# Optimization experiments

Measured on AMD Instinct MI355X. Metric: run time of the kernel, lower is better.

The kernel has to match this reference:

```python
import jax, jax.numpy as jnp
import numpy as np

# nqsystems=8 grouped sites, physical dim d=2^ncontraq=16,
# state bond r=64, layer (unitary MPO) bond rl=16, operator MPO bond ro=4,
# nlsystems=1 pre-contracted circuit layer.
NQ, R, D, RL, RO, NL = 8, 64, 16, 16, 4, 1


def setup_inputs() -> dict:
    key = jax.random.key(0)
    k1, k2, k3 = jax.random.split(key, 3)
    # scale so contractions stay O(1) numerically
    state = jax.random.normal(k1, (NQ, R, D, R), jnp.float32) / np.float32(np.sqrt(R * D))
    layer = jax.random.normal(k2, (NL, NQ, RL, D, D, RL), jnp.float32) / np.float32(np.sqrt(RL * D))
    operator = jax.random.normal(k3, (NQ, RO, D, D, RO), jnp.float32) / np.float32(np.sqrt(RO * D))
    return {"state": state, "layer": layer, "operator": operator}


def reference(state, layer, operator):
    """<psi| U^dagger O U |psi> contracted site-by-site along the TT chain.

    state:    [nq, r, d, r]        TT cores of |psi>
    layer:    [nl, nq, rl, d, d, rl]  TT-operator cores of the circuit layer (nl=1)
    operator: [nq, ro, d, d, ro]   TT-operator cores of the observable
    """
    r, rl, ro = state.shape[1], layer.shape[3], operator.shape[1]
    # open-boundary closure: boundary vectors = e0 on every bond
    env0 = jnp.zeros((r, rl, ro, rl, r), state.dtype).at[0, 0, 0, 0, 0].set(1.0)
    U = layer[0]  # nlsystems == 1

    def step(env, cores):
        S, Uq, Oq = cores
        # tt_dagger: conj + transpose physical indices (0,2,1,3)
        Ud = jnp.conj(Uq).transpose(0, 2, 1, 3)
        # env axes: a=bra-state bond, l=bra-layer bond, o=operator bond,
        #           m=ket-layer bond, b=ket-state bond
        t = jnp.einsum('alomb,aiA->lombiA', env, jnp.conj(S))   # bra state core
        t = jnp.einsum('lombiA,lijL->ombAjL', t, Ud)            # U^dagger core
        t = jnp.einsum('ombAjL,ojkO->mbALkO', t, Oq)            # observable core
        t = jnp.einsum('mbALkO,mksM->bALOsM', t, Uq)            # U core
        t = jnp.einsum('bALOsM,bsB->ALOMB', t, S)               # ket state core
        return t, None

    env, _ = jax.lax.scan(step, env0, (state, U, operator))
    return env[0, 0, 0, 0, 0]
```

## Files before the change

### kernel.cpp

```cpp
#include <hip/hip_runtime.h>


typedef __attribute__((ext_vector_type(8))) short bf16x8;
typedef __attribute__((ext_vector_type(8))) _Float16 f16x8;
typedef __attribute__((ext_vector_type(4))) float f32x4;
typedef __attribute__((ext_vector_type(4))) unsigned short us4;

static __device__ __forceinline__ unsigned short f2bf(float x) {
    union { float f; unsigned u; } a; a.f = x;
    return (unsigned short)((a.u + 0x7FFF + ((a.u >> 16) & 1)) >> 16);
}
static __device__ __forceinline__ float bf2f(unsigned short h) {
    union { unsigned u; float f; } a; a.u = (unsigned)h << 16; return a.f;
}
static __device__ __forceinline__ unsigned split2(float x) {
    unsigned short h = f2bf(x);
    unsigned short l = f2bf(x - bf2f(h));
    return (unsigned)h | ((unsigned)l << 16);
}
static __device__ __forceinline__ void split2_pair(float x0, float x1,
                                                   unsigned& o0, unsigned& o1) {
    unsigned hh, ll;
    asm("v_cvt_pk_bf16_f32 %0, %1, %2" : "=v"(hh) : "v"(x0), "v"(x1));
    union { unsigned u; float f; } c0, c1;
    c0.u = hh << 16;
    c1.u = hh & 0xffff0000u;
    float r0 = x0 - c0.f, r1 = x1 - c1.f;
    asm("v_cvt_pk_bf16_f32 %0, %1, %2" : "=v"(ll) : "v"(r0), "v"(r1));
    asm("v_perm_b32 %0, %1, %2, %3" : "=v"(o0) : "v"(ll), "v"(hh), "s"(0x05040100));
    asm("v_perm_b32 %0, %1, %2, %3" : "=v"(o1) : "v"(ll), "v"(hh), "s"(0x07060302));
}
static __device__ __forceinline__ unsigned short f2h_bits(float x) {
    union { _Float16 h; unsigned short u; } c; c.h = (_Float16)x; return c.u;
}
static __device__ __forceinline__ float h2f_bits(unsigned short u) {
    union { unsigned short u; _Float16 h; } c; c.u = u; return (float)c.h;
}
static __device__ __forceinline__ void gl_lds16(const unsigned short* g,
                                                unsigned short* l) {
    __builtin_amdgcn_global_load_lds(
        (const __attribute__((address_space(1))) unsigned int*)g,
        (__attribute__((address_space(3))) unsigned int*)l, 16, 0, 0);
}

__global__ void write_diag_kernel(float* out, float v) {
    if (threadIdx.x == 0 && blockIdx.x == 0) out[0] = v;
}
__global__ void zero_out(float* o) {
    if (threadIdx.x == 0 && blockIdx.x == 0) o[0] = 0.0f;
}

__global__ void prep_apack(const float* __restrict__ layer,
                           unsigned short* __restrict__ Ap2,
                           unsigned short* __restrict__ Ap4) {
    int idx = blockIdx.x * 256 + threadIdx.x;
    int q = idx >> 13, k0 = (idx >> 10) & 7, mt = (idx >> 6) & 15, lane = idx & 63;
    int quad = lane >> 4, r = lane & 15;
    unsigned short h2[8], l2[8], h4[8], l4[8];
#pragma unroll
    for (int j = 0; j < 8; j++) {
        int k = k0 * 32 + quad * 8 + j;
        int m = mt * 16 + r;
        float v2 = layer[(size_t)q * 65536 +
                         (size_t)((((k >> 4) * 16 + (m >> 4)) * 16 + (k & 15)) * 16 + (m & 15))];
        float v4 = layer[(size_t)q * 65536 +
                         (size_t)((((k >> 4) * 16 + (k & 15)) * 16 + (m >> 4)) * 16 + (m & 15))];
        h2[j] = f2h_bits(v2); l2[j] = f2h_bits(v2 - h2f_bits(h2[j]));
        h4[j] = f2h_bits(v4); l4[j] = f2h_bits(v4 - h2f_bits(h4[j]));
    }
    size_t base = ((size_t)((q * 8 + k0) * 16 + mt) * 2) * 512 + lane * 8;
    *(us4*)(Ap2 + base)       = *(us4*)&h2[0];
    *(us4*)(Ap2 + base + 4)   = *(us4*)&h2[4];
    *(us4*)(Ap2 + base + 512) = *(us4*)&l2[0];
    *(us4*)(Ap2 + base + 516) = *(us4*)&l2[4];
    *(us4*)(Ap4 + base)       = *(us4*)&h4[0];
    *(us4*)(Ap4 + base + 4)   = *(us4*)&h4[4];
    *(us4*)(Ap4 + base + 512) = *(us4*)&l4[0];
    *(us4*)(Ap4 + base + 516) = *(us4*)&l4[4];
}

__global__ void prep_spack1(const float* __restrict__ state,
                            unsigned short* __restrict__ Sp1) {
    int idx = blockIdx.x * 256 + threadIdx.x;
    int q = idx >> 13, c = (idx >> 11) & 3, k0 = (idx >> 10) & 1,
        mt = (idx >> 6) & 15, lane = idx & 63;
    int quad = lane >> 4, lr = lane & 15;
    unsigned short h[8], l[8];
#pragma unroll
    for (int j = 0; j < 8; j++) {
        int k = k0 * 32 + quad * 8 + j;
        float v = state[(size_t)q * 65536 + (size_t)(k * 16 + mt) * 64 + c * 16 + lr];
        h[j] = f2bf(v); l[j] = f2bf(v - bf2f(h[j]));
    }
    size_t base = (size_t)(q * 4 + c) * 32768 + ((size_t)(k0 * 16 + mt) * 2) * 512 + lane * 8;
    *(us4*)(Sp1 + base)       = *(us4*)&h[0];
    *(us4*)(Sp1 + base + 4)   = *(us4*)&h[4];
    *(us4*)(Sp1 + base + 512) = *(us4*)&l[0];
    *(us4*)(Sp1 + base + 516) = *(us4*)&l[4];
}

__global__ void prep_spack5(const float* __restrict__ state,
                            unsigned short* __restrict__ Sp5) {
    int idx = blockIdx.x * 256 + threadIdx.x;
    int q = idx >> 13, k0 = (idx >> 8) & 31, mt = (idx >> 6) & 3, lane = idx & 63;
    int quad = lane >> 4, lr = lane & 15;
    unsigned short h[8], l[8];
#pragma unroll
    for (int j = 0; j < 8; j++) {
        int k = k0 * 32 + quad * 8 + j;
        int s = k >> 6, b = k & 63;
        float v = state[(size_t)q * 65536 + (size_t)(b * 16 + s) * 64 + mt * 16 + lr];
        h[j] = f2bf(v); l[j] = f2bf(v - bf2f(h[j]));
    }
    size_t base = (size_t)q * 131072 + ((size_t)(k0 * 4 + mt) * 2) * 512 + lane * 8;
    *(us4*)(Sp5 + base)       = *(us4*)&h[0];
    *(us4*)(Sp5 + base + 4)   = *(us4*)&h[4];
    *(us4*)(Sp5 + base + 512) = *(us4*)&l[0];
    *(us4*)(Sp5 + base + 516) = *(us4*)&l[4];
}

__global__ void prep_opack3(const float* __restrict__ oper,
                            unsigned short* __restrict__ Op3) {
    int idx = blockIdx.x * 256 + threadIdx.x;
    int q = idx >> 9, k0 = (idx >> 8) & 1, mt = (idx >> 6) & 3, lane = idx & 63;
    int quad = lane >> 4, lr = lane & 15;
    unsigned short h[8], l[8];
#pragma unroll
    for (int j = 0; j < 8; j++) {
        int k = k0 * 32 + quad * 8 + j;
        int m = mt * 16 + lr;
        float v = oper[(size_t)q * 4096 + (size_t)(k * 16 + (m & 15)) * 4 + (m >> 4)];
        h[j] = f2h_bits(v); l[j] = f2h_bits(v - h2f_bits(h[j]));
    }
    size_t base = (size_t)q * 8192 + ((size_t)(k0 * 4 + mt) * 2) * 512 + lane * 8;
    *(us4*)(Op3 + base)       = *(us4*)&h[0];
    *(us4*)(Op3 + base + 4)   = *(us4*)&h[4];
    *(us4*)(Op3 + base + 512) = *(us4*)&l[0];
    *(us4*)(Op3 + base + 516) = *(us4*)&l[4];
}

__global__ void env_split_k(const float* __restrict__ env, unsigned* __restrict__ envS) {
    int t = blockIdx.x * 256 + threadIdx.x;
    float4 v = ((const float4*)env)[t];
    uint4 o;
    o.x = split2(v.x); o.y = split2(v.y); o.z = split2(v.z); o.w = split2(v.w);
    ((uint4*)envS)[t] = o;
}

__global__ void s0_g2(const float* __restrict__ state, const float* __restrict__ layer,
                      float* __restrict__ g2) {
    int t = blockIdx.x * 256 + threadIdx.x;
    int A = t >> 8, j = (t >> 4) & 15, L = t & 15;
    float s = 0;
    for (int i = 0; i < 16; i++) s += state[i * 64 + A] * layer[(j * 16 + i) * 16 + L];
    g2[t] = s;
}
__global__ void s0_g3(const float* __restrict__ g2, const float* __restrict__ oper,
                      float* __restrict__ g3) {
    int t = blockIdx.x * 256 + threadIdx.x;
    int A = t >> 10, L = (t >> 6) & 15, k = (t >> 2) & 15, O = t & 3;
    float s = 0;
    for (int j = 0; j < 16; j++) s += g2[A * 256 + j * 16 + L] * oper[(j * 16 + k) * 4 + O];
    g3[t] = s;
}
__global__ void s0_g4(const float* __restrict__ g3, const float* __restrict__ layer,
                      float* __restrict__ g4) {
    int t = blockIdx.x * 256 + threadIdx.x;
    int A = t >> 14, L = (t >> 10) & 15, O = (t >> 8) & 3, sp = (t >> 4) & 15, M = t & 15;
    float s = 0;
    for (int k = 0; k < 16; k++)
        s += g3[A * 1024 + L * 64 + k * 4 + O] * layer[(k * 16 + sp) * 16 + M];
    g4[t] = s;
}
__global__ void s0_env(const float* __restrict__ g4, const float* __restrict__ state,
                       float* __restrict__ env) {
    int t = blockIdx.x * 256 + threadIdx.x;
    int A = t >> 16, L = (t >> 12) & 15, O = (t >> 10) & 3, M = (t >> 6) & 15, B = t & 63;
    float s = 0;
    for (int sp = 0; sp < 16; sp++)
        s += g4[A * 16384 + L * 1024 + O * 256 + sp * 16 + M] * state[sp * 64 + B];
    env[(size_t)(L * 64 + O * 16 + M) * 4096 + A * 64 + B] = s;
}

__global__ void s7_c1(const float* __restrict__ state, const float* __restrict__ layer,
                      float* __restrict__ c1) {
    int t = blockIdx.x * 256 + threadIdx.x;
    int l = t >> 10, a = (t >> 4) & 63, j = t & 15;
    float s = 0;
    for (int i = 0; i < 16; i++)
        s += state[7 * 65536 + (a * 16 + i) * 64] * layer[7 * 65536 + ((l * 16 + j) * 16 + i) * 16];
    c1[t] = s;
}
__global__ void s7_c2(const float* __restrict__ c1, const float* __restrict__ oper,
                      float* __restrict__ c2) {
    int t = blockIdx.x * 256 + threadIdx.x;
    int o = t >> 14, l = (t >> 10) & 15, a = (t >> 4) & 63, k = t & 15;
    float s = 0;
    for (int j = 0; j < 16; j++)
        s += c1[l * 1024 + a * 16 + j] * oper[7 * 4096 + ((o * 16 + j) * 16 + k) * 4];
    c2[t] = s;
}
__global__ void s7_c3(const float* __restrict__ c2, const float* __restrict__ layer,
                      float* __restrict__ c3) {
    int t = blockIdx.x * 256 + threadIdx.x;
    int m = t >> 16, o = (t >> 14) & 3, l = (t >> 10) & 15, a = (t >> 4) & 63, sp = t & 15;
    float s = 0;
    for (int k = 0; k < 16; k++)
        s += c2[o * 16384 + l * 1024 + a * 16 + k] *
             layer[7 * 65536 + ((m * 16 + k) * 16 + sp) * 16];
    c3[t] = s;
}
__global__ void prep_sv(const float* __restrict__ state, float* __restrict__ sv) {
    int t = blockIdx.x * 256 + threadIdx.x;
    sv[t] = state[7 * 65536 + t * 64];
}
__global__ __launch_bounds__(256) void s7_fused(const float* __restrict__ env,
                                                const float* __restrict__ c3,
                                                const float* __restrict__ sv,
                                                float* __restrict__ out) {
    __shared__ float c3s[1024], svs[1024], red[256];
    int t = threadIdx.x;
    int n0 = blockIdx.x * 64;
    int l = n0 >> 12, o = (n0 >> 10) & 3, m = (n0 >> 6) & 15;
    const float* c3b = c3 + m * 65536 + o * 16384 + l * 1024;
    const float* eb  = env + (size_t)blockIdx.x * 4096;
    for (int i = t; i < 1024; i += 256) { c3s[i] = c3b[i]; svs[i] = sv[i]; }
    __syncthreads();
    float s = 0;
    int b = t & 63, ag = t >> 6;
#pragma unroll
    for (int g = 0; g < 16; g++) {
        int a = ag * 16 + g;
        float e = eb[a * 64 + b];
        float w = 0;
#pragma unroll
        for (int sp = 0; sp < 16; sp++) w += c3s[a * 16 + sp] * svs[b * 16 + sp];
        s += e * w;
    }
    red[t] = s; __syncthreads();
    for (int off = 128; off; off >>= 1) { if (t < off) red[t] += red[t + off]; __syncthreads(); }
    if (t == 0) atomicAdd(out, red[0]);
}

__global__ __launch_bounds__(256) void gemm_g1(const unsigned* __restrict__ envS,
                                               const unsigned short* __restrict__ Sp1,
                                               unsigned short* __restrict__ t1,
                                               float scale) {
    __shared__ unsigned Bt[32 * 65];
    const int tid = threadIdx.x, lane = tid & 63, wave = tid >> 6;
    const int quad = lane >> 4, lr = lane & 15;
    const int cc = blockIdx.x >> 10, rid = blockIdx.x & 1023;
    const int l = rid >> 6, o = (rid >> 4) & 3, m2 = rid & 15;

    f32x4 acc[4][4];
#pragma unroll
    for (int i = 0; i < 4; i++)
#pragma unroll
        for (int j = 0; j < 4; j++)
#pragma unroll
            for (int r = 0; r < 4; r++) acc[i][j][r] = 0.0f;

    const unsigned* Bv = envS + (size_t)rid * 4096;
    const unsigned short* Sp1c = Sp1 + (size_t)cc * 32768;
    uint4 ur[2];
    auto load_tile = [&](int k0) {
        const uint4* src = (const uint4*)(Bv + k0 * 2048);
        ur[0] = src[tid];
        ur[1] = src[256 + tid];
    };
    auto store_tile = [&]() {
#pragma unroll
        for (int v = 0; v < 2; v++) {
            int e = v * 256 + tid;
            unsigned* p = &Bt[(e >> 4) * 65 + (e & 15) * 4];
            p[0] = ur[v].x; p[1] = ur[v].y; p[2] = ur[v].z; p[3] = ur[v].w;
        }
    };

    bf16x8 ahb[2][4], alb[2][4];
    auto loadA = [&](int k0, int buf) {
#pragma unroll
        for (int mt = 0; mt < 4; mt++) {
            int gmt = wave * 4 + mt;
            const unsigned short* ap = Sp1c + ((size_t)(k0 * 16 + gmt) * 2) * 512 + lane * 8;
            ahb[buf][mt] = *(const bf16x8*)ap;
            alb[buf][mt] = *(const bf16x8*)(ap + 512);
        }
    };

    load_tile(0);
    loadA(0, 0);
    store_tile();
#pragma unroll
    for (int k0 = 0; k0 < 2; k0++) {
        __syncthreads();
        if (k0 + 1 < 2) { load_tile(k0 + 1); loadA(k0 + 1, 1); }
#pragma unroll
        for (int nt = 0; nt < 4; nt++) {
            int nl = nt * 16 + lr;
            bf16x8 bh, bl;
#pragma unroll
            for (int j = 0; j < 8; j++) {
                unsigned u = Bt[(quad * 8 + j) * 65 + nl];
                bh[j] = (short)(u & 0xffffu);
                bl[j] = (short)(u >> 16);
            }
#pragma unroll
            for (int mt = 0; mt < 4; mt++) {
                acc[mt][nt] = __builtin_amdgcn_mfma_f32_16x16x32_bf16(ahb[k0][mt], bh, acc[mt][nt], 0, 0, 0);
                acc[mt][nt] = __builtin_amdgcn_mfma_f32_16x16x32_bf16(ahb[k0][mt], bl, acc[mt][nt], 0, 0, 0);
                acc[mt][nt] = __builtin_amdgcn_mfma_f32_16x16x32_bf16(alb[k0][mt], bh, acc[mt][nt], 0, 0, 0);
            }
        }
        __syncthreads();
        if (k0 + 1 < 2) store_tile();
    }

#pragma unroll
    for (int nt = 0; nt < 4; nt++) {
        int b = nt * 16 + lr;
#pragma unroll
        for (int r = 0; r < 4; r++) {
            int a4 = quad * 4 + r;
            us4 w;
#pragma unroll
            for (int mt = 0; mt < 4; mt++) w[mt] = f2h_bits(acc[mt][nt][r] * scale);
            size_t addr = (size_t)cc * 16777216 +
                          (size_t)(o * 256 + m2 * 16 + a4) * 16384 +
                          (size_t)(l * 2 + (wave >> 1)) * 512 + b * 8 + (wave & 1) * 4;
            *(us4*)(t1 + addr) = w;
        }
    }
}

__global__ __launch_bounds__(256) void gemm_g2(const unsigned short* __restrict__ Bp,
                                               const unsigned short* __restrict__ Ap,
                                               unsigned short* __restrict__ Co) {
    __shared__ __align__(16) unsigned short Bs[16384];
    const int tid = threadIdx.x, lane = tid & 63, wave = tid >> 6;
    const int quad = lane >> 4, lr = lane & 15;
    const int cc = blockIdx.x >> 10, rid = blockIdx.x & 1023;
    const int o = rid >> 8, m2 = (rid >> 4) & 15, a4 = rid & 15;
    const unsigned short* pb = Bp + (size_t)blockIdx.x * 16384;
    unsigned short* Cb = Co + (size_t)cc * 16777216;

#pragma unroll
    for (int i = 0; i < 8; i++)
        gl_lds16(pb + i * 2048 + tid * 8, Bs + i * 2048 + wave * 512);

    f32x4 acc[4][4];
#pragma unroll
    for (int i = 0; i < 4; i++)
#pragma unroll
        for (int j = 0; j < 4; j++)
#pragma unroll
            for (int r = 0; r < 4; r++) acc[i][j][r] = 0.0f;

    f16x8 ah[3][4];
    auto loadA = [&](int k0, int buf) {
#pragma unroll
        for (int mt = 0; mt < 4; mt++) {
            int gmt = wave * 4 + mt;
            ah[buf][mt] = *(const f16x8*)(Ap + ((size_t)(k0 * 16 + gmt) * 2) * 512 + lane * 8);
        }
    };
    loadA(0, 0);
    loadA(1, 1);

    asm volatile("s_waitcnt vmcnt(0)" ::: "memory");
    __syncthreads();

#pragma unroll
    for (int k0 = 0; k0 < 8; k0++) {
        if (k0 + 2 < 8) loadA(k0 + 2, (k0 + 2) % 3);
        f16x8 bfr[4];
#pragma unroll
        for (int nt = 0; nt < 4; nt++)
            bfr[nt] = *(const f16x8*)(Bs + (k0 * 4 + quad) * 512 + (nt * 16 + lr) * 8);
#pragma unroll
        for (int nt = 0; nt < 4; nt++)
#pragma unroll
            for (int mt = 0; mt < 4; mt++)
                acc[mt][nt] = __builtin_amdgcn_mfma_f32_16x16x32_f16(
                    ah[k0 % 3][mt], bfr[nt], acc[mt][nt], 0, 0, 0);
    }

#pragma unroll
    for (int nt = 0; nt < 4; nt++) {
        int b = nt * 16 + lr;
#pragma unroll
        for (int r = 0; r < 4; r++) {
            int L = quad * 4 + r;
            us4 w;
#pragma unroll
            for (int mt = 0; mt < 4; mt++) w[mt] = f2h_bits(acc[mt][nt][r]);
            size_t addr = (size_t)(L * 256 + m2 * 16 + a4) * 4096 +
                          (size_t)(o * 2 + (wave >> 1)) * 512 + b * 8 + (wave & 1) * 4;
            *(us4*)(Cb + addr) = w;
        }
    }
}

__global__ __launch_bounds__(256) void gemm_g45(const unsigned short* __restrict__ T2,
                                                const unsigned short* __restrict__ Op3q,
                                                const unsigned short* __restrict__ Ap4,
                                                const unsigned short* __restrict__ Sp5,
                                                float* __restrict__ env,
                                                unsigned* __restrict__ envSo,
                                                int A0, float inv, int wf32) {
    __shared__ __align__(16) unsigned short Bs[16384];
    __shared__ unsigned SL[4 * 16 * 68];
    const int tid = threadIdx.x, lane = tid & 63, wave = tid >> 6;
    const int quad = lane >> 4, lr = lane & 15;
    const int cc = blockIdx.x >> 10, rid = blockIdx.x & 1023;
    const int low = rid & 7, O2 = (rid >> 3) & 3, g = rid >> 5;
    const int panel = g * 8 + low;
    const int L = panel >> 4, a4 = panel & 15;
    const unsigned short* T2c = T2 + (size_t)cc * 16777216;
    const int b8 = (wave * 16 + lr) * 8;

    f16x8 ah[3][4];
    auto loadA = [&](int k0, int buf) {
#pragma unroll
        for (int mt = 0; mt < 4; mt++) {
            int gmt = wave * 4 + mt;
            ah[buf][mt] = *(const f16x8*)(Ap4 + ((size_t)(k0 * 16 + gmt) * 2) * 512 + lane * 8);
        }
    };
    loadA(0, 0);
    loadA(1, 1);

    {
        f16x8 oh0 = *(const f16x8*)(Op3q + (size_t)(O2 * 2) * 512 + lane * 8);
        f16x8 oh1 = *(const f16x8*)(Op3q + (size_t)((4 + O2) * 2) * 512 + lane * 8);
        f16x8 tb[5][2];
        auto loadT2 = [&](int m2, int buf) {
            const unsigned short* pp = T2c + (size_t)(L * 256 + m2 * 16 + a4) * 4096;
            tb[buf][0] = *(const f16x8*)(pp + (quad << 9) + b8);
            tb[buf][1] = *(const f16x8*)(pp + ((4 + quad) << 9) + b8);
        };
        loadT2(0, 0); loadT2(1, 1); loadT2(2, 2); loadT2(3, 3);
#pragma unroll
        for (int m2 = 0; m2 < 16; m2++) {
            if (m2 + 4 < 16) loadT2(m2 + 4, (m2 + 4) % 5);
            f32x4 a3;
            a3[0] = a3[1] = a3[2] = a3[3] = 0.0f;
            a3 = __builtin_amdgcn_mfma_f32_16x16x32_f16(oh0, tb[m2 % 5][0], a3, 0, 0, 0);
            a3 = __builtin_amdgcn_mfma_f32_16x16x32_f16(oh1, tb[m2 % 5][1], a3, 0, 0, 0);
            us4 w;
#pragma unroll
            for (int r = 0; r < 4; r++) w[r] = f2h_bits(a3[r]);
            *(us4*)(Bs + (m2 * 2 + (quad >> 1)) * 512 + b8 + (quad & 1) * 4) = w;
        }
    }
    __syncthreads();

    f32x4 acc[4][4];
#pragma unroll
    for (int i = 0; i < 4; i++)
#pragma unroll
        for (int j = 0; j < 4; j++)
#pragma unroll
            for (int r = 0; r < 4; r++) acc[i][j][r] = 0.0f;

#pragma unroll
    for (int k0 = 0; k0 < 8; k0++) {
        if (k0 + 2 < 8) loadA(k0 + 2, (k0 + 2) % 3);
        f16x8 bfr[4];
#pragma unroll
        for (int nt = 0; nt < 4; nt++)
            bfr[nt] = *(const f16x8*)(Bs + (k0 * 4 + quad) * 512 + (nt * 16 + lr) * 8);
#pragma unroll
        for (int nt = 0; nt < 4; nt++)
#pragma unroll
            for (int mt = 0; mt < 4; mt++)
                acc[mt][nt] = __builtin_amdgcn_mfma_f32_16x16x32_f16(
                    ah[k0 % 3][mt], bfr[nt], acc[mt][nt], 0, 0, 0);
    }

    unsigned* myslab = SL + wave * (16 * 68);
    f32x4 acc5[4];
#pragma unroll
    for (int nt = 0; nt < 4; nt++)
#pragma unroll
        for (int r = 0; r < 4; r++) acc5[nt][r] = 0.0f;

    bf16x8 s5h[2][4], s5l[2][4];
    auto loadS5 = [&](int step, int buf) {
        int kg = (wave * 4 + (step >> 1)) * 2 + (step & 1);
#pragma unroll
        for (int nt = 0; nt < 4; nt++) {
            const unsigned short* bp = Sp5 + ((size_t)(kg * 4 + nt) * 2) * 512 + lane * 8;
            s5h[buf][nt] = *(const bf16x8*)bp;
            s5l[buf][nt] = *(const bf16x8*)(bp + 512);
        }
    };
    loadS5(0, 0);

#pragma unroll
    for (int mtp = 0; mtp < 4; mtp++) {
#pragma unroll
        for (int nt = 0; nt < 4; nt++) {
            unsigned o0, o1, o2, o3;
            split2_pair(acc[mtp][nt][0], acc[mtp][nt][1], o0, o1);
            split2_pair(acc[mtp][nt][2], acc[mtp][nt][3], o2, o3);
            myslab[(quad * 4 + 0) * 68 + nt * 16 + lr] = o0;
            myslab[(quad * 4 + 1) * 68 + nt * 16 + lr] = o1;
            myslab[(quad * 4 + 2) * 68 + nt * 16 + lr] = o2;
            myslab[(quad * 4 + 3) * 68 + nt * 16 + lr] = o3;
        }
        asm volatile("s_waitcnt lgkmcnt(0)" ::: "memory");
#pragma unroll
        for (int h = 0; h < 2; h++) {
            const int step = mtp * 2 + h;
            const unsigned* sp = &myslab[lr * 68 + h * 32 + quad * 8];
            uint4 u0 = *(const uint4*)sp;
            uint4 u1 = *(const uint4*)(sp + 4);
            bf16x8 th, tl;
            th[0] = (short)(u0.x & 0xffff); tl[0] = (short)(u0.x >> 16);
            th[1] = (short)(u0.y & 0xffff); tl[1] = (short)(u0.y >> 16);
            th[2] = (short)(u0.z & 0xffff); tl[2] = (short)(u0.z >> 16);
            th[3] = (short)(u0.w & 0xffff); tl[3] = (short)(u0.w >> 16);
            th[4] = (short)(u1.x & 0xffff); tl[4] = (short)(u1.x >> 16);
            th[5] = (short)(u1.y & 0xffff); tl[5] = (short)(u1.y >> 16);
            th[6] = (short)(u1.z & 0xffff); tl[6] = (short)(u1.z >> 16);
            th[7] = (short)(u1.w & 0xffff); tl[7] = (short)(u1.w >> 16);
            if (step + 1 < 8) loadS5(step + 1, (step + 1) & 1);
#pragma unroll
            for (int nt = 0; nt < 4; nt++) {
                acc5[nt] = __builtin_amdgcn_mfma_f32_16x16x32_bf16(th, s5h[step & 1][nt], acc5[nt], 0, 0, 0);
                acc5[nt] = __builtin_amdgcn_mfma_f32_16x16x32_bf16(th, s5l[step & 1][nt], acc5[nt], 0, 0, 0);
                acc5[nt] = __builtin_amdgcn_mfma_f32_16x16x32_bf16(tl, s5h[step & 1][nt], acc5[nt], 0, 0, 0);
            }
        }
    }

    __syncthreads();
    float* red = (float*)SL;
#pragma unroll
    for (int nt = 0; nt < 4; nt++)
#pragma unroll
        for (int r = 0; r < 4; r++)
            red[wave * 1088 + (quad * 4 + r) * 68 + nt * 16 + lr] = acc5[nt][r];
    __syncthreads();
    float wv[4];
#pragma unroll
    for (int r = 0; r < 4; r++) {
        int M2 = quad * 4 + r, Bc = wave * 16 + lr;
        float v = red[M2 * 68 + Bc] + red[1088 + M2 * 68 + Bc] +
                  red[2176 + M2 * 68 + Bc] + red[3264 + M2 * 68 + Bc];
        wv[r] = v * inv;
    }
    unsigned s0p, s1p, s2p, s3p;
    split2_pair(wv[0], wv[1], s0p, s1p);
    split2_pair(wv[2], wv[3], s2p, s3p);
    unsigned sp4[4] = {s0p, s1p, s2p, s3p};
#pragma unroll
    for (int r = 0; r < 4; r++) {
        int M2 = quad * 4 + r, Bc = wave * 16 + lr;
        size_t idx = (size_t)(L * 64 + O2 * 16 + M2) * 4096 + (A0 + cc * 16 + a4) * 64 + Bc;
        envSo[idx] = sp4[r];
        if (wf32) env[idx] = wv[r];
    }
}

extern "C" void kernel_launch(void* const* d_in, const int* in_sizes, int n_in,
                              void* d_out, int out_size, void* d_ws, size_t ws_size,
                              hipStream_t stream) {
    const float* state = (const float*)d_in[0];
    const float* layer = (const float*)d_in[1];
    const float* oper  = (const float*)d_in[2];
    float* out = (float*)d_out;

    const size_t need = 16777216ull * 4 + 33554432ull * 4 + 3ull * 4194304ull * 4 +
                        (4ull * 1048576ull + 65536ull) * 2ull + 4096ull;
    if (ws_size < need) {
        write_diag_kernel<<<1, 64, 0, stream>>>(out, (float)ws_size);
        return;
    }
    float* F    = (float*)d_ws;
    unsigned* P = (unsigned*)(F + 16777216);
    unsigned* envS0 = (unsigned*)(P + 33554432);
    float* envB = (float*)(envS0 + 4194304);
    unsigned* envS1 = (unsigned*)(envB + 4194304);
    unsigned short* Ap2 = (unsigned short*)(envS1 + 4194304);
    unsigned short* Ap4 = Ap2 + 1048576;
    unsigned short* Sp1 = Ap4 + 1048576;
    unsigned short* Sp5 = Sp1 + 1048576;
    unsigned short* Op3 = Sp5 + 1048576;
    float* sv = (float*)(Op3 + 65536);
    float* SCR = F;
    unsigned short* T1 = (unsigned short*)P;
    unsigned short* T2 = (unsigned short*)F;

    prep_apack<<<256, 256, 0, stream>>>(layer, Ap2, Ap4);
    prep_spack1<<<256, 256, 0, stream>>>(state, Sp1);
    prep_spack5<<<256, 256, 0, stream>>>(state, Sp5);
    prep_opack3<<<16, 256, 0, stream>>>(oper, Op3);
    prep_sv<<<4, 256, 0, stream>>>(state, sv);

    s0_g2<<<64, 256, 0, stream>>>(state, layer, SCR);
    s0_g3<<<256, 256, 0, stream>>>(SCR, oper, SCR + 16384);
    s0_g4<<<4096, 256, 0, stream>>>(SCR + 16384, layer, SCR + 81920);
    s0_env<<<16384, 256, 0, stream>>>(SCR + 81920, state, envB);
    env_split_k<<<4096, 256, 0, stream>>>(envB, envS1);

    for (int q = 1; q < 7; q++) {
        unsigned* einS  = (q & 1) ? envS1 : envS0;
        unsigned* eoutS = (q & 1) ? envS0 : envS1;
        float scl = (float)(1u << (16 + 2 * q));
        float inv = 1.0f / scl;
        int wf32 = (q == 6) ? 1 : 0;
        for (int p = 0; p < 2; p++) {
            gemm_g1<<<2048, 256, 0, stream>>>(
                einS, Sp1 + (size_t)(q * 4 + p * 2) * 32768, T1, scl);
            gemm_g2<<<2048, 256, 0, stream>>>(
                T1, Ap2 + (size_t)q * 131072, T2);
            gemm_g45<<<2048, 256, 0, stream>>>(
                T2, Op3 + (size_t)q * 8192, Ap4 + (size_t)q * 131072,
                Sp5 + (size_t)q * 131072, envB, eoutS, p * 32, inv, wf32);
        }
    }

    s7_c1<<<64, 256, 0, stream>>>(state, layer, SCR);
    s7_c2<<<256, 256, 0, stream>>>(SCR, oper, SCR + 16384);
    s7_c3<<<4096, 256, 0, stream>>>(SCR + 16384, layer, SCR + 81920);
    zero_out<<<1, 64, 0, stream>>>(out);
    s7_fused<<<1024, 256, 0, stream>>>(envB, SCR + 81920, sv, out);
}
```

Measured before the change: 1.396 ms.

## Co-schedule second-pass g1 with first-pass g2 in one fused launch

Moves the bodies of gemm_g1 and gemm_g2 into device functions and adds a combined kernel whose even blocks run g2 for pass p=0 and whose odd blocks run g1 for pass p=1. T1 is double-buffered so the two passes do not collide. The aim is to overlap the memory-heavy g1 with the MFMA-heavy g2 and to remove one launch per q. In exchange the combined kernel uses the larger shared-memory footprint (32 KB), which may lower occupancy for the g1 blocks, and the second T1 buffer adds workspace pressure.

```diff
diff --git a/kernel.cpp b/kernel.cpp
--- a/kernel.cpp
+++ b/kernel.cpp
@@ -242,14 +242,15 @@
     if (t == 0) atomicAdd(out, red[0]);
 }
 
-__global__ __launch_bounds__(256) void gemm_g1(const unsigned* __restrict__ envS,
+static __device__ __forceinline__ void g1_body(int bid, void* smem,
+                                               const unsigned* __restrict__ envS,
                                                const unsigned short* __restrict__ Sp1,
                                                unsigned short* __restrict__ t1,
                                                float scale) {
-    __shared__ unsigned Bt[32 * 65];
+    unsigned* Bt = (unsigned*)smem;
     const int tid = threadIdx.x, lane = tid & 63, wave = tid >> 6;
     const int quad = lane >> 4, lr = lane & 15;
-    const int cc = blockIdx.x >> 10, rid = blockIdx.x & 1023;
+    const int cc = bid >> 10, rid = bid & 1023;
     const int l = rid >> 6, o = (rid >> 4) & 3, m2 = rid & 15;
 
     f32x4 acc[4][4];
@@ -333,72 +334,103 @@
     }
 }
 
+__global__ __launch_bounds__(256) void gemm_g1(const unsigned* __restrict__ envS,
+                                               const unsigned short* __restrict__ Sp1,
+                                               unsigned short* __restrict__ t1,
+                                               float scale) {
+    __shared__ unsigned Bt[32 * 65];
+    g1_body(blockIdx.x, Bt, envS, Sp1, t1, scale);
+}
+
+static __device__ __forceinline__ void g2_body(int bid, void* smem,
+                                               const unsigned short* __restrict__ Bp,
+                                               const unsigned short* __restrict__ Ap,
+                                               unsigned short* __restrict__ Co) {
+    unsigned short* Bs = (unsigned short*)smem;
+    const int tid = threadIdx.x, lane = tid & 63, wave = tid >> 6;
+    const int quad = lane >> 4, lr = lane & 15;
+    const int cc = bid >> 10, rid = bid & 1023;
+    const int o = rid >> 8, m2 = (rid >> 4) & 15, a4 = rid & 15;
+    const unsigned short* pb = Bp + (size_t)bid * 16384;
+    unsigned short* Cb = Co + (size_t)cc * 16777216;
+
+#pragma unroll
+    for (int i = 0; i < 8; i++)
+        gl_lds16(pb + i * 2048 + tid * 8, Bs + i * 2048 + wave * 512);
+
+    f32x4 acc[4][4];
+#pragma unroll
+    for (int i = 0; i < 4; i++)
+#pragma unroll
+        for (int j = 0; j < 4; j++)
+#pragma unroll
+            for (int r = 0; r < 4; r++) acc[i][j][r] = 0.0f;
+
+    f16x8 ah[3][4];
+    auto loadA = [&](int k0, int buf) {
+#pragma unroll
+        for (int mt = 0; mt < 4; mt++) {
+            int gmt = wave * 4 + mt;
+            ah[buf][mt] = *(const f16x8*)(Ap + ((size_t)(k0 * 16 + gmt) * 2) * 512 + lane * 8);
+        }
+    };
+    loadA(0, 0);
+    loadA(1, 1);
+
+    asm volatile("s_waitcnt vmcnt(0)" ::: "memory");
+    __syncthreads();
+
+#pragma unroll
+    for (int k0 = 0; k0 < 8; k0++) {
+        if (k0 + 2 < 8) loadA(k0 + 2, (k0 + 2) % 3);
+        f16x8 bfr[4];
+#pragma unroll
+        for (int nt = 0; nt < 4; nt++)
+            bfr[nt] = *(const f16x8*)(Bs + (k0 * 4 + quad) * 512 + (nt * 16 + lr) * 8);
+#pragma unroll
+        for (int nt = 0; nt < 4; nt++)
+#pragma unroll
+            for (int mt = 0; mt < 4; mt++)
+                acc[mt][nt] = __builtin_amdgcn_mfma_f32_16x16x32_f16(
+                    ah[k0 % 3][mt], bfr[nt], acc[mt][nt], 0, 0, 0);
+    }
+
+#pragma unroll
+    for (int nt = 0; nt < 4; nt++) {
+        int b = nt * 16 + lr;
+#pragma unroll
+        for (int r = 0; r < 4; r++) {
+            int L = quad * 4 + r;
+            us4 w;
+#pragma unroll
+            for (int mt = 0; mt < 4; mt++) w[mt] = f2h_bits(acc[mt][nt][r]);
+            size_t addr = (size_t)(L * 256 + m2 * 16 + a4) * 4096 +
+                          (size_t)(o * 2 + (wave >> 1)) * 512 + b * 8 + (wave & 1) * 4;
+            *(us4*)(Cb + addr) = w;
+        }
+    }
+}
+
 __global__ __launch_bounds__(256) void gemm_g2(const unsigned short* __restrict__ Bp,
                                                const unsigned short* __restrict__ Ap,
                                                unsigned short* __restrict__ Co) {
     __shared__ __align__(16) unsigned short Bs[16384];
-    const int tid = threadIdx.x, lane = tid & 63, wave = tid >> 6;
-    const int quad = lane >> 4, lr = lane & 15;
-    const int cc = blockIdx.x >> 10, rid = blockIdx.x & 1023;
-    const int o = rid >> 8, m2 = (rid >> 4) & 15, a4 = rid & 15;
-    const unsigned short* pb = Bp + (size_t)blockIdx.x * 16384;
-    unsigned short* Cb = Co + (size_t)cc * 16777216;
-
-#pragma unroll
-    for (int i = 0; i < 8; i++)
-        gl_lds16(pb + i * 2048 + tid * 8, Bs + i * 2048 + wave * 512);
-
-    f32x4 acc[4][4];
-#pragma unroll
-    for (int i = 0; i < 4; i++)
-#pragma unroll
-        for (int j = 0; j < 4; j++)
-#pragma unroll
-            for (int r = 0; r < 4; r++) acc[i][j][r] = 0.0f;
-
-    f16x8 ah[3][4];
-    auto loadA = [&](int k0, int buf) {
-#pragma unroll
-        for (int mt = 0; mt < 4; mt++) {
-            int gmt = wave * 4 + mt;
-            ah[buf][mt] = *(const f16x8*)(Ap + ((size_t)(k0 * 16 + gmt) * 2) * 512 + lane * 8);
-        }
-    };
-    loadA(0, 0);
-    loadA(1, 1);
-
-    asm volatile("s_waitcnt vmcnt(0)" ::: "memory");
-    __syncthreads();
-
-#pragma unroll
-    for (int k0 = 0; k0 < 8; k0++) {
-        if (k0 + 2 < 8) loadA(k0 + 2, (k0 + 2) % 3);
-        f16x8 bfr[4];
-#pragma unroll
-        for (int nt = 0; nt < 4; nt++)
-            bfr[nt] = *(const f16x8*)(Bs + (k0 * 4 + quad) * 512 + (nt * 16 + lr) * 8);
-#pragma unroll
-        for (int nt = 0; nt < 4; nt++)
-#pragma unroll
-            for (int mt = 0; mt < 4; mt++)
-                acc[mt][nt] = __builtin_amdgcn_mfma_f32_16x16x32_f16(
-                    ah[k0 % 3][mt], bfr[nt], acc[mt][nt], 0, 0, 0);
-    }
-
-#pragma unroll
-    for (int nt = 0; nt < 4; nt++) {
-        int b = nt * 16 + lr;
-#pragma unroll
-        for (int r = 0; r < 4; r++) {
-            int L = quad * 4 + r;
-            us4 w;
-#pragma unroll
-            for (int mt = 0; mt < 4; mt++) w[mt] = f2h_bits(acc[mt][nt][r]);
-            size_t addr = (size_t)(L * 256 + m2 * 16 + a4) * 4096 +
-                          (size_t)(o * 2 + (wave >> 1)) * 512 + b * 8 + (wave & 1) * 4;
-            *(us4*)(Cb + addr) = w;
-        }
-    }
+    g2_body(blockIdx.x, Bs, Bp, Ap, Co);
+}
+
+__global__ __launch_bounds__(256) void fused_g2_g1(
+        const unsigned short* __restrict__ Bp,
+        const unsigned short* __restrict__ Ap,
+        unsigned short* __restrict__ Co,
+        const unsigned* __restrict__ envS,
+        const unsigned short* __restrict__ Sp1b,
+        unsigned short* __restrict__ t1,
+        float scale) {
+    __shared__ __align__(16) unsigned char smem[32768];
+    if (blockIdx.x & 1)
+        g1_body(blockIdx.x >> 1, smem, envS, Sp1b, t1, scale);
+    else
+        g2_body(blockIdx.x >> 1, smem, Bp, Ap, Co);
 }
 
 __global__ __launch_bounds__(256) void gemm_g45(const unsigned short* __restrict__ T2,
@@ -590,7 +622,8 @@
     unsigned short* Op3 = Sp5 + 1048576;
     float* sv = (float*)(Op3 + 65536);
     float* SCR = F;
-    unsigned short* T1 = (unsigned short*)P;
+    unsigned short* T1p0 = (unsigned short*)P;
+    unsigned short* T1p1 = T1p0 + 33554432;
     unsigned short* T2 = (unsigned short*)F;
 
     prep_apack<<<256, 256, 0, stream>>>(layer, Ap2, Ap4);
@@ -611,15 +644,19 @@
         float scl = (float)(1u << (16 + 2 * q));
         float inv = 1.0f / scl;
         int wf32 = (q == 6) ? 1 : 0;
-        for (int p = 0; p < 2; p++) {
-            gemm_g1<<<2048, 256, 0, stream>>>(
-                einS, Sp1 + (size_t)(q * 4 + p * 2) * 32768, T1, scl);
-            gemm_g2<<<2048, 256, 0, stream>>>(
-                T1, Ap2 + (size_t)q * 131072, T2);
-            gemm_g45<<<2048, 256, 0, stream>>>(
-                T2, Op3 + (size_t)q * 8192, Ap4 + (size_t)q * 131072,
-                Sp5 + (size_t)q * 131072, envB, eoutS, p * 32, inv, wf32);
-        }
+        gemm_g1<<<2048, 256, 0, stream>>>(
+            einS, Sp1 + (size_t)(q * 4 + 0) * 32768, T1p0, scl);
+        fused_g2_g1<<<4096, 256, 0, stream>>>(
+            T1p0, Ap2 + (size_t)q * 131072, T2,
+            einS, Sp1 + (size_t)(q * 4 + 2) * 32768, T1p1, scl);
+        gemm_g45<<<2048, 256, 0, stream>>>(
+            T2, Op3 + (size_t)q * 8192, Ap4 + (size_t)q * 131072,
+            Sp5 + (size_t)q * 131072, envB, eoutS, 0, inv, wf32);
+        gemm_g2<<<2048, 256, 0, stream>>>(
+            T1p1, Ap2 + (size_t)q * 131072, T2);
+        gemm_g45<<<2048, 256, 0, stream>>>(
+            T2, Op3 + (size_t)q * 8192, Ap4 + (size_t)q * 131072,
+            Sp5 + (size_t)q * 131072, envB, eoutS, 32, inv, wf32);
     }
 
     s7_c1<<<64, 256, 0, stream>>>(state, layer, SCR);
```

New measurement: 1.381 ms. No clear change (-1.1%).
